# Kernel tuning notes

Measured on AMD Instinct MI355X. Metric: run time of the kernel, lower is better.

The kernel has to match this reference:

```python
import jax, jax.numpy as jnp
import numpy as np

N_NODES = 100000
N_EDGES = 1600000
D = 64
N_LAYERS = 5
N_GRAPHS = 256


def setup_inputs() -> dict:
    key = jax.random.key(0)
    ks = jax.random.split(key, 12)
    x = jax.random.normal(ks[0], (N_NODES, D), dtype=jnp.float32)
    edge_index = jax.random.randint(ks[1], (2, N_EDGES), 0, N_NODES, dtype=jnp.int64)
    batch = jnp.sort(jax.random.randint(ks[2], (N_NODES,), 0, N_GRAPHS, dtype=jnp.int64))
    s = 1.0 / np.sqrt(D)
    # stacked GINConv MLP params: Linear(D,D) -> ReLU -> Linear(D,D), per layer
    Ws1 = jax.random.uniform(ks[3], (N_LAYERS, D, D), jnp.float32, -s, s)
    bs1 = jax.random.uniform(ks[4], (N_LAYERS, D), jnp.float32, -s, s)
    Ws2 = jax.random.uniform(ks[5], (N_LAYERS, D, D), jnp.float32, -s, s)
    bs2 = jax.random.uniform(ks[6], (N_LAYERS, D), jnp.float32, -s, s)
    # final readout MLP: Linear(D,D) -> ReLU -> Linear(D,D)
    mW1 = jax.random.uniform(ks[7], (D, D), jnp.float32, -s, s)
    mb1 = jax.random.uniform(ks[8], (D,), jnp.float32, -s, s)
    mW2 = jax.random.uniform(ks[9], (D, D), jnp.float32, -s, s)
    mb2 = jax.random.uniform(ks[10], (D,), jnp.float32, -s, s)
    return {"x": x, "edge_index": edge_index, "batch": batch,
            "Ws1": Ws1, "bs1": bs1, "Ws2": Ws2, "bs2": bs2,
            "mW1": mW1, "mb1": mb1, "mW2": mW2, "mb2": mb2}


def reference(x, edge_index, batch, Ws1, bs1, Ws2, bs2, mW1, mb1, mW2, mb2):
    src, dst = edge_index[0], edge_index[1]
    h = x
    for l in range(N_LAYERS):
        # GINConv (eps=0): MLP(h + sum_{j in N(i)} h_j)
        agg = jax.ops.segment_sum(h[src], dst, num_segments=N_NODES)
        z = h + agg
        z = jax.nn.relu(z @ Ws1[l] + bs1[l])
        h = z @ Ws2[l] + bs2[l]
    # global mean pool over graphs
    sums = jax.ops.segment_sum(h, batch, num_segments=N_GRAPHS)
    cnts = jax.ops.segment_sum(jnp.ones((h.shape[0],), h.dtype), batch, num_segments=N_GRAPHS)
    pooled = sums / jnp.maximum(cnts, 1.0)[:, None]
    # readout MLP
    out = jax.nn.relu(pooled @ mW1 + mb1) @ mW2 + mb2
    return out
```

## Files before the change

kernel.cpp:

```cpp
#include <hip/hip_runtime.h>
#include <hip/hip_bf16.h>

#define N_NODES 100000
#define N_EDGES 1600000
#define DIM 64
#define N_LAYERS 5
#define N_GRAPHS 256

#define NB2 391
#define BSH 8
#define BMSK 255
#define SUBCAP2 4608
#define CAP2 6400
#define DUMMY N_NODES
#define TILE 3200
#define NTILE 500
#define MTILES (N_NODES / 16)

#define CVT_BLOCKS 6250
#define PREPACK_BLOCKS 40
#define SETUP_BLOCKS (CVT_BLOCKS + PREPACK_BLOCKS + 1)

typedef __attribute__((ext_vector_type(8))) short short8;
typedef __attribute__((ext_vector_type(4))) float float4v;

__device__ __forceinline__ unsigned short f2bf(float f) {
    unsigned int u = __float_as_uint(f);
    unsigned int r = (u + 0x7fffu + ((u >> 16) & 1u)) >> 16;
    return (unsigned short)r;
}
__device__ __forceinline__ float bf2f(unsigned short b) {
    return __uint_as_float(((unsigned int)b) << 16);
}

__global__ __launch_bounds__(256) void setup_kernel(
    const float4* __restrict__ x, ushort4* __restrict__ hb,
    const float* __restrict__ Ws1, const float* __restrict__ Ws2,
    unsigned short* __restrict__ wpk, int* __restrict__ bcursor,
    unsigned short* __restrict__ hA, unsigned short* __restrict__ hB) {
    const int b = blockIdx.x;
    const int tid = threadIdx.x;
    if (b < CVT_BLOCKS) {
        int i = b * 256 + tid;
        float4 v = x[i];
        ushort4 o;
        o.x = f2bf(v.x); o.y = f2bf(v.y); o.z = f2bf(v.z); o.w = f2bf(v.w);
        hb[i] = o;
    } else if (b < CVT_BLOCKS + PREPACK_BLOCKS) {
        int t = (b - CVT_BLOCKS) * 256 + tid;
        int lane = t & 63;
        int frag = (t >> 6) & 31;
        int l = t >> 11;
        int kf = frag & 1;
        int nt = (frag >> 1) & 3;
        int split = (frag >> 3) & 1;
        int mat = (frag >> 4) & 1;
        const float* W = (mat ? Ws2 : Ws1) + (size_t)l * DIM * DIM;
        unsigned short outv[8];
#pragma unroll
        for (int j = 0; j < 8; ++j) {
            int k = kf * 32 + ((lane >> 4) << 3) + j;
            int n = nt * 16 + (lane & 15);
            float v = W[k * DIM + n];
            unsigned short hi = f2bf(v);
            outv[j] = split ? f2bf(v - bf2f(hi)) : hi;
        }
        ushort4* dst = (ushort4*)(wpk + ((size_t)(l * 32 + frag) * 64 + lane) * 8);
        dst[0] = make_ushort4(outv[0], outv[1], outv[2], outv[3]);
        dst[1] = make_ushort4(outv[4], outv[5], outv[6], outv[7]);
    } else {
        for (int l = tid; l < NB2; l += 256) bcursor[l] = 0;
        if (tid < DIM) {
            hA[(size_t)DUMMY * DIM + tid] = 0;
            hB[(size_t)DUMMY * DIM + tid] = 0;
        }
    }
}

__global__ __launch_bounds__(256) void bin_kernel(
    const int* __restrict__ src, const int* __restrict__ dst,
    int* __restrict__ bcursor, int* __restrict__ pairbuf) {
    __shared__ int hcnt[NB2];
    __shared__ int gbase[NB2];
    __shared__ int lcur[NB2];
    const int tid = threadIdx.x;
    const int base = blockIdx.x * TILE;

    for (int l = tid; l < NB2; l += 256) { hcnt[l] = 0; lcur[l] = 0; }
    __syncthreads();
    for (int j = tid; j < TILE; j += 256) {
        int d = dst[base + j];
        atomicAdd(&hcnt[d >> BSH], 1);
    }
    __syncthreads();
    for (int l = tid; l < NB2; l += 256)
        gbase[l] = atomicAdd(&bcursor[l], hcnt[l]);
    __syncthreads();
    for (int j = tid; j < TILE; j += 256) {
        int s = src[base + j];
        int d = dst[base + j];
        int b = d >> BSH;
        int r = atomicAdd(&lcur[b], 1);
        int pos = gbase[b] + r;
        if (pos < SUBCAP2) pairbuf[b * SUBCAP2 + pos] = (s << BSH) | (d & BMSK);
    }
}

__global__ __launch_bounds__(512) void csr_kernel(
    const int* __restrict__ bcursor, const int* __restrict__ pairbuf,
    int* __restrict__ esrc, int2* __restrict__ meta) {
    __shared__ int lcnt[256];
    __shared__ int loff[256];
    __shared__ int lcur[256];
    __shared__ int s2[256];
    const int b = blockIdx.x;
    const int tid = threadIdx.x;
    int ec = bcursor[b];
    if (ec > SUBCAP2) ec = SUBCAP2;
    const int* pp = pairbuf + b * SUBCAP2;

    if (tid < 256) lcnt[tid] = 0;
    __syncthreads();
    for (int j = tid; j < ec; j += 512) atomicAdd(&lcnt[pp[j] & BMSK], 1);
    __syncthreads();

    if (tid < 256) s2[tid] = (lcnt[tid] + 7) & ~7;
    __syncthreads();
    for (int off = 1; off < 256; off <<= 1) {
        int v = (tid >= off && tid < 256) ? s2[tid - off] : 0;
        __syncthreads();
        if (tid < 256) s2[tid] += v;
        __syncthreads();
    }
    if (tid < 256) {
        int c = (lcnt[tid] + 7) & ~7;
        int exc = s2[tid] - c;
        loff[tid] = exc;
        lcur[tid] = exc;
    }
    __syncthreads();

    int* eb = esrc + (size_t)b * CAP2;
    for (int l = tid; l < 256; l += 512) {
        int st = loff[l];
        int cn = lcnt[l];
        int cp = (cn + 7) & ~7;
        int node = b * 256 + l;
        if (node < N_NODES) meta[node] = make_int2(b * CAP2 + st, cp);
        for (int j = cn; j < cp; ++j) eb[st + j] = DUMMY;
    }
    __syncthreads();

    for (int j = tid; j < ec; j += 512) {
        int p = pp[j];
        int pos = atomicAdd(&lcur[p & BMSK], 1);
        eb[pos] = p >> BSH;
    }
}

__device__ __forceinline__ void acc8(float* acc, uint4 v) {
    acc[0] += __uint_as_float(v.x << 16);
    acc[1] += __uint_as_float(v.x & 0xffff0000u);
    acc[2] += __uint_as_float(v.y << 16);
    acc[3] += __uint_as_float(v.y & 0xffff0000u);
    acc[4] += __uint_as_float(v.z << 16);
    acc[5] += __uint_as_float(v.z & 0xffff0000u);
    acc[6] += __uint_as_float(v.w << 16);
    acc[7] += __uint_as_float(v.w & 0xffff0000u);
}

typedef const __attribute__((address_space(1))) void* as1cv;
typedef __attribute__((address_space(3))) void* as3v;
__device__ __forceinline__ void gload16(const void* g, void* l) {
    __builtin_amdgcn_global_load_lds((as1cv)g, (as3v)l, 16, 0, 0);
}

__global__ __launch_bounds__(256) void agg_kernel(
    const unsigned short* __restrict__ hin, unsigned short* __restrict__ z,
    const int2* __restrict__ meta, const int* __restrict__ esrc, int n_nodes) {
    __shared__ char scratch[4][4096];
    const int lane = threadIdx.x & 63;
    const int wv = threadIdx.x >> 6;
    const int grp = lane >> 3;
    const int sub = lane & 7;
    const int wave_id = (blockIdx.x * blockDim.x + threadIdx.x) >> 6;
    const int n_waves = (gridDim.x * blockDim.x) >> 6;
    char* ring = scratch[wv];
    const char* hb = (const char*)hin;

    for (int ii = wave_id; 2 * ii < n_nodes; ii += n_waves) {
        const int iA = 2 * ii;
        const int iB = iA + 1;
        const int2 mA = meta[iA];
        const int2 mB = meta[iB];
        const float selfA = bf2f(hin[(size_t)iA * DIM + lane]);
        const float selfB = bf2f(hin[(size_t)iB * DIM + lane]);
        const int nA = mA.y, nB = mB.y;
        const int* eA = esrc + mA.x + grp;
        const int* eB = esrc + mB.x + grp;
        const int nb = ((nA > nB) ? nA : nB) >> 3;

        float accA[8] = {0.f, 0.f, 0.f, 0.f, 0.f, 0.f, 0.f, 0.f};
        float accB[8] = {0.f, 0.f, 0.f, 0.f, 0.f, 0.f, 0.f, 0.f};

        if (nb > 0) {
            int o;
            o = (0 < nA) ? 0 : 0;
            int ia0 = eA[o]; ia0 = (0 < nA) ? ia0 : DUMMY;
            int ib0 = eB[o]; ib0 = (0 < nB) ? ib0 : DUMMY;
            o = (8 < nA) ? 8 : 0;
            int ia1 = eA[o]; ia1 = (8 < nA) ? ia1 : DUMMY;
            o = (8 < nB) ? 8 : 0;
            int ib1 = eB[o]; ib1 = (8 < nB) ? ib1 : DUMMY;
            asm volatile("s_waitcnt lgkmcnt(0)" ::: "memory");
            gload16(hb + ((size_t)(unsigned)ia0 << 7) + (sub << 4), ring);
            gload16(hb + ((size_t)(unsigned)ib0 << 7) + (sub << 4), ring + 2048);
            if (nb > 1) {
                gload16(hb + ((size_t)(unsigned)ia1 << 7) + (sub << 4), ring + 1024);
                gload16(hb + ((size_t)(unsigned)ib1 << 7) + (sub << 4), ring + 3072);
            }
            asm volatile("" ::: "memory");
            int t8 = 16;
            int oA = (t8 < nA) ? t8 : 0;
            int oB = (t8 < nB) ? t8 : 0;
            int nxA = eA[oA]; nxA = (t8 < nA) ? nxA : DUMMY;
            int nxB = eB[oB]; nxB = (t8 < nB) ? nxB : DUMMY;

            for (int b = 0; b < nb; ++b) {
                if (b + 1 < nb) asm volatile("s_waitcnt vmcnt(4)" ::: "memory");
                else            asm volatile("s_waitcnt vmcnt(2)" ::: "memory");
                const int s = (b & 1) << 10;
                uint4 va = *(const uint4*)(ring + s + lane * 16);
                uint4 vb = *(const uint4*)(ring + 2048 + s + lane * 16);
                acc8(accA, va);
                acc8(accB, vb);
                if (b + 2 < nb) {
                    asm volatile("s_waitcnt lgkmcnt(0)" ::: "memory");
                    gload16(hb + ((size_t)(unsigned)nxA << 7) + (sub << 4), ring + s);
                    gload16(hb + ((size_t)(unsigned)nxB << 7) + (sub << 4), ring + 2048 + s);
                    asm volatile("" ::: "memory");
                    t8 = 8 * (b + 3);
                    oA = (t8 < nA) ? t8 : 0;
                    oB = (t8 < nB) ? t8 : 0;
                    nxA = eA[oA]; nxA = (t8 < nA) ? nxA : DUMMY;
                    nxB = eB[oB]; nxB = (t8 < nB) ? nxB : DUMMY;
                }
            }
        }

        float* zbA = (float*)ring;
        float* zbB = (float*)(ring + 2048);
        *((float4*)&zbA[grp * 64 + sub * 8 + 0]) = make_float4(accA[0], accA[1], accA[2], accA[3]);
        *((float4*)&zbA[grp * 64 + sub * 8 + 4]) = make_float4(accA[4], accA[5], accA[6], accA[7]);
        *((float4*)&zbB[grp * 64 + sub * 8 + 0]) = make_float4(accB[0], accB[1], accB[2], accB[3]);
        *((float4*)&zbB[grp * 64 + sub * 8 + 4]) = make_float4(accB[4], accB[5], accB[6], accB[7]);
        __builtin_amdgcn_wave_barrier();
        float zA = selfA, zB = selfB;
#pragma unroll
        for (int g = 0; g < 8; ++g) {
            zA += zbA[g * 64 + lane];
            zB += zbB[g * 64 + lane];
        }
        z[(size_t)iA * DIM + lane] = f2bf(zA);
        z[(size_t)iB * DIM + lane] = f2bf(zB);
        __builtin_amdgcn_wave_barrier();
    }
}

__device__ __forceinline__ short8 load_frag(const unsigned short* __restrict__ wl, int frag, int lane) {
    union { uint4 u; short8 s; } c;
    c.u = *(const uint4*)(wl + ((size_t)(frag * 64 + lane)) * 8);
    return c.s;
}

__device__ __forceinline__ void split8(const float* v, short8& hi, short8& lo) {
#pragma unroll
    for (int j = 0; j < 8; ++j) {
        unsigned short h = f2bf(v[j]);
        hi[j] = (short)h;
        lo[j] = (short)f2bf(v[j] - bf2f(h));
    }
}

__global__ __launch_bounds__(256) void mlp_mfma_kernel(
    const unsigned short* __restrict__ z, unsigned short* __restrict__ hout,
    const unsigned short* __restrict__ wl,
    const float* __restrict__ b1, const float* __restrict__ b2) {
    __shared__ float tbuf[4][16][68];
    const int lane = threadIdx.x & 63;
    const int wv = threadIdx.x >> 6;
    const int m = lane & 15;
    const int quad = lane >> 4;
    const int wave_id = (blockIdx.x * blockDim.x + threadIdx.x) >> 6;
    const int n_waves = (gridDim.x * blockDim.x) >> 6;

    float b1v[4], b2v[4];
#pragma unroll
    for (int nt = 0; nt < 4; ++nt) {
        b1v[nt] = b1[nt * 16 + m];
        b2v[nt] = b2[nt * 16 + m];
    }

    for (int tile = wave_id; tile < MTILES; tile += n_waves) {
        const int node0 = tile * 16;

        short8 a1[2];
#pragma unroll
        for (int kf = 0; kf < 2; ++kf) {
            union { uint4 u; short8 s; } c;
            c.u = *(const uint4*)(z + ((size_t)(node0 + m)) * DIM + kf * 32 + quad * 8);
            a1[kf] = c.s;
        }

        float4v acc1[4] = {};
#pragma unroll
        for (int nt = 0; nt < 4; ++nt) {
#pragma unroll
            for (int kf = 0; kf < 2; ++kf) {
                short8 bhi = load_frag(wl, ((0 * 2 + 0) * 4 + nt) * 2 + kf, lane);
                short8 blo = load_frag(wl, ((0 * 2 + 1) * 4 + nt) * 2 + kf, lane);
                acc1[nt] = __builtin_amdgcn_mfma_f32_16x16x32_bf16(a1[kf], bhi, acc1[nt], 0, 0, 0);
                acc1[nt] = __builtin_amdgcn_mfma_f32_16x16x32_bf16(a1[kf], blo, acc1[nt], 0, 0, 0);
            }
        }

#pragma unroll
        for (int nt = 0; nt < 4; ++nt) {
#pragma unroll
            for (int r = 0; r < 4; ++r) {
                float tv = acc1[nt][r] + b1v[nt];
                tbuf[wv][quad * 4 + r][nt * 16 + m] = fmaxf(tv, 0.f);
            }
        }
        __builtin_amdgcn_wave_barrier();

        short8 a2hi[2], a2lo[2];
#pragma unroll
        for (int kf = 0; kf < 2; ++kf) {
            const float4* tp = (const float4*)&tbuf[wv][m][kf * 32 + quad * 8];
            float4 t0 = tp[0];
            float4 t1 = tp[1];
            float v[8] = {t0.x, t0.y, t0.z, t0.w, t1.x, t1.y, t1.z, t1.w};
            split8(v, a2hi[kf], a2lo[kf]);
        }
        __builtin_amdgcn_wave_barrier();

        float4v acc2[4] = {};
#pragma unroll
        for (int nt = 0; nt < 4; ++nt) {
#pragma unroll
            for (int kf = 0; kf < 2; ++kf) {
                short8 bhi = load_frag(wl, ((1 * 2 + 0) * 4 + nt) * 2 + kf, lane);
                short8 blo = load_frag(wl, ((1 * 2 + 1) * 4 + nt) * 2 + kf, lane);
                acc2[nt] = __builtin_amdgcn_mfma_f32_16x16x32_bf16(a2hi[kf], bhi, acc2[nt], 0, 0, 0);
                acc2[nt] = __builtin_amdgcn_mfma_f32_16x16x32_bf16(a2hi[kf], blo, acc2[nt], 0, 0, 0);
                acc2[nt] = __builtin_amdgcn_mfma_f32_16x16x32_bf16(a2lo[kf], bhi, acc2[nt], 0, 0, 0);
            }
        }

#pragma unroll
        for (int nt = 0; nt < 4; ++nt) {
#pragma unroll
            for (int r = 0; r < 4; ++r) {
                float o = acc2[nt][r] + b2v[nt];
                hout[((size_t)(node0 + quad * 4 + r)) * DIM + nt * 16 + m] = f2bf(o);
            }
        }
    }
}

__global__ __launch_bounds__(256) void pool_mlp_kernel(
    const unsigned short* __restrict__ h, const int* __restrict__ batch,
    const float* __restrict__ mW1, const float* __restrict__ mb1,
    const float* __restrict__ mW2, const float* __restrict__ mb2,
    float* __restrict__ out, int n_nodes) {
    __shared__ float part[4][DIM];
    const int g = blockIdx.x;
    const int lane = threadIdx.x & 63;
    const int w = threadIdx.x >> 6;

    int lo = 0, hi = n_nodes;
    while (lo < hi) {
        int mid = (lo + hi) >> 1;
        if (batch[mid] < g) lo = mid + 1; else hi = mid;
    }
    const int s0 = lo;
    hi = n_nodes;
    while (lo < hi) {
        int mid = (lo + hi) >> 1;
        if (batch[mid] < g + 1) lo = mid + 1; else hi = mid;
    }
    const int e0 = lo;

    float acc = 0.f;
    int i = s0 + w;
    for (; i + 12 < e0; i += 16) {
        float v0 = bf2f(h[i * DIM + lane]);
        float v1 = bf2f(h[(i + 4) * DIM + lane]);
        float v2 = bf2f(h[(i + 8) * DIM + lane]);
        float v3 = bf2f(h[(i + 12) * DIM + lane]);
        acc += (v0 + v1) + (v2 + v3);
    }
    for (; i < e0; i += 4) acc += bf2f(h[i * DIM + lane]);
    part[w][lane] = acc;
    __syncthreads();

    if (w == 0) {
        acc = (part[0][lane] + part[1][lane]) + (part[2][lane] + part[3][lane]);
        float cntf = (float)(e0 - s0);
        acc /= fmaxf(cntf, 1.f);

        float t = mb1[lane];
#pragma unroll
        for (int d = 0; d < DIM; ++d) {
            float zd = __shfl(acc, d);
            t = fmaf(zd, mW1[d * DIM + lane], t);
        }
        t = fmaxf(t, 0.f);
        float o = mb2[lane];
#pragma unroll
        for (int d = 0; d < DIM; ++d) {
            float rd = __shfl(t, d);
            o = fmaf(rd, mW2[d * DIM + lane], o);
        }
        out[g * DIM + lane] = o;
    }
}

extern "C" void kernel_launch(void* const* d_in, const int* in_sizes, int n_in,
                              void* d_out, int out_size, void* d_ws, size_t ws_size,
                              hipStream_t stream) {
    const float* x   = (const float*)d_in[0];
    const int*   ei  = (const int*)d_in[1];
    const int*   bat = (const int*)d_in[2];
    const float* Ws1 = (const float*)d_in[3];
    const float* bs1 = (const float*)d_in[4];
    const float* Ws2 = (const float*)d_in[5];
    const float* bs2 = (const float*)d_in[6];
    const float* mW1 = (const float*)d_in[7];
    const float* mb1 = (const float*)d_in[8];
    const float* mW2 = (const float*)d_in[9];
    const float* mb2 = (const float*)d_in[10];
    float* out = (float*)d_out;

    char* ws = (char*)d_ws;
    size_t off = 0;
    auto alloc = [&](size_t bytes) {
        void* p = ws + off;
        off += (bytes + 255) & ~(size_t)255;
        return p;
    };
    int*  esrc    = (int*)alloc((size_t)NB2 * CAP2 * 4);
    int2* meta    = (int2*)alloc((size_t)N_NODES * 8);
    unsigned short* hbfA = (unsigned short*)alloc(((size_t)N_NODES + 1) * DIM * 2);
    unsigned short* hbfB = (unsigned short*)alloc(((size_t)N_NODES + 1) * DIM * 2);
    int*  bcursor = (int*)alloc((size_t)NB2 * 4);
    unsigned short* wpk = (unsigned short*)alloc((size_t)N_LAYERS * 32 * 64 * 8 * 2);
    int*   pairbuf = (int*)alloc((size_t)NB2 * SUBCAP2 * 4);
    unsigned short* zbig = (unsigned short*)alloc((size_t)N_NODES * DIM * 2);

    const int* src = ei;
    const int* dst = ei + N_EDGES;

    setup_kernel<<<SETUP_BLOCKS, 256, 0, stream>>>(
        (const float4*)x, (ushort4*)hbfA, Ws1, Ws2, wpk, bcursor, hbfA, hbfB);

    bin_kernel<<<NTILE, 256, 0, stream>>>(src, dst, bcursor, pairbuf);
    csr_kernel<<<NB2, 512, 0, stream>>>(bcursor, pairbuf, esrc, meta);

    const unsigned short* hin = hbfA;
    unsigned short* hout = hbfB;
    for (int l = 0; l < N_LAYERS; ++l) {
        agg_kernel<<<2048, 256, 0, stream>>>(hin, zbig, meta, esrc, N_NODES);
        mlp_mfma_kernel<<<2048, 256, 0, stream>>>(zbig, hout,
                                                  wpk + (size_t)l * 32 * 64 * 8,
                                                  bs1 + (size_t)l * DIM,
                                                  bs2 + (size_t)l * DIM);
        hin = hout;
        hout = (hout == hbfA) ? hbfB : hbfA;
    }
    pool_mlp_kernel<<<N_GRAPHS, 256, 0, stream>>>(hin, bat, mW1, mb1, mW2, mb2, out, N_NODES);
}
```

Baseline: 371.4 us.

## Fuse neighbor aggregation and GIN MLP into one per-wave kernel

Merges the aggregation kernel and the MFMA MLP kernel into a single kernel. Each wave aggregates 16 nodes into an XOR-swizzled LDS tile and then runs both linear layers on it, so the bf16 z buffer no longer round-trips through global memory and one launch per layer is dropped. The LDS layout for the intermediate ReLU buffer is also swizzled instead of padded. The trade-off is that gather latency and MFMA work are now serialized inside each wave, the grid shrinks to 1536 blocks, and register pressure is higher, which may reduce occupancy for the latency-bound gather.

Result: slower. 484.4 us (+30.4%).

```diff
diff --git a/kernel.cpp b/kernel.cpp
--- a/kernel.cpp
+++ b/kernel.cpp
@@ -175,124 +175,39 @@
     __builtin_amdgcn_global_load_lds((as1cv)g, (as3v)l, 16, 0, 0);
 }
 
-__global__ __launch_bounds__(256) void agg_kernel(
-    const unsigned short* __restrict__ hin, unsigned short* __restrict__ z,
-    const int2* __restrict__ meta, const int* __restrict__ esrc, int n_nodes) {
-    __shared__ char scratch[4][4096];
+__device__ __forceinline__ short8 load_frag(const unsigned short* __restrict__ wl, int frag, int lane) {
+    union { uint4 u; short8 s; } c;
+    c.u = *(const uint4*)(wl + ((size_t)(frag * 64 + lane)) * 8);
+    return c.s;
+}
+
+__device__ __forceinline__ void split8(const float* v, short8& hi, short8& lo) {
+#pragma unroll
+    for (int j = 0; j < 8; ++j) {
+        unsigned short h = f2bf(v[j]);
+        hi[j] = (short)h;
+        lo[j] = (short)f2bf(v[j] - bf2f(h));
+    }
+}
+
+__global__ __launch_bounds__(256) void fused_wave_kernel(
+    const unsigned short* __restrict__ hin, unsigned short* __restrict__ hout,
+    const int2* __restrict__ meta, const int* __restrict__ esrc,
+    const unsigned short* __restrict__ wl,
+    const float* __restrict__ b1, const float* __restrict__ b2) {
+    __shared__ char ringbuf[4][4096];
+    __shared__ unsigned short ztbuf[4][16 * DIM];
     const int lane = threadIdx.x & 63;
     const int wv = threadIdx.x >> 6;
     const int grp = lane >> 3;
     const int sub = lane & 7;
-    const int wave_id = (blockIdx.x * blockDim.x + threadIdx.x) >> 6;
-    const int n_waves = (gridDim.x * blockDim.x) >> 6;
-    char* ring = scratch[wv];
-    const char* hb = (const char*)hin;
-
-    for (int ii = wave_id; 2 * ii < n_nodes; ii += n_waves) {
-        const int iA = 2 * ii;
-        const int iB = iA + 1;
-        const int2 mA = meta[iA];
-        const int2 mB = meta[iB];
-        const float selfA = bf2f(hin[(size_t)iA * DIM + lane]);
-        const float selfB = bf2f(hin[(size_t)iB * DIM + lane]);
-        const int nA = mA.y, nB = mB.y;
-        const int* eA = esrc + mA.x + grp;
-        const int* eB = esrc + mB.x + grp;
-        const int nb = ((nA > nB) ? nA : nB) >> 3;
-
-        float accA[8] = {0.f, 0.f, 0.f, 0.f, 0.f, 0.f, 0.f, 0.f};
-        float accB[8] = {0.f, 0.f, 0.f, 0.f, 0.f, 0.f, 0.f, 0.f};
-
-        if (nb > 0) {
-            int o;
-            o = (0 < nA) ? 0 : 0;
-            int ia0 = eA[o]; ia0 = (0 < nA) ? ia0 : DUMMY;
-            int ib0 = eB[o]; ib0 = (0 < nB) ? ib0 : DUMMY;
-            o = (8 < nA) ? 8 : 0;
-            int ia1 = eA[o]; ia1 = (8 < nA) ? ia1 : DUMMY;
-            o = (8 < nB) ? 8 : 0;
-            int ib1 = eB[o]; ib1 = (8 < nB) ? ib1 : DUMMY;
-            asm volatile("s_waitcnt lgkmcnt(0)" ::: "memory");
-            gload16(hb + ((size_t)(unsigned)ia0 << 7) + (sub << 4), ring);
-            gload16(hb + ((size_t)(unsigned)ib0 << 7) + (sub << 4), ring + 2048);
-            if (nb > 1) {
-                gload16(hb + ((size_t)(unsigned)ia1 << 7) + (sub << 4), ring + 1024);
-                gload16(hb + ((size_t)(unsigned)ib1 << 7) + (sub << 4), ring + 3072);
-            }
-            asm volatile("" ::: "memory");
-            int t8 = 16;
-            int oA = (t8 < nA) ? t8 : 0;
-            int oB = (t8 < nB) ? t8 : 0;
-            int nxA = eA[oA]; nxA = (t8 < nA) ? nxA : DUMMY;
-            int nxB = eB[oB]; nxB = (t8 < nB) ? nxB : DUMMY;
-
-            for (int b = 0; b < nb; ++b) {
-                if (b + 1 < nb) asm volatile("s_waitcnt vmcnt(4)" ::: "memory");
-                else            asm volatile("s_waitcnt vmcnt(2)" ::: "memory");
-                const int s = (b & 1) << 10;
-                uint4 va = *(const uint4*)(ring + s + lane * 16);
-                uint4 vb = *(const uint4*)(ring + 2048 + s + lane * 16);
-                acc8(accA, va);
-                acc8(accB, vb);
-                if (b + 2 < nb) {
-                    asm volatile("s_waitcnt lgkmcnt(0)" ::: "memory");
-                    gload16(hb + ((size_t)(unsigned)nxA << 7) + (sub << 4), ring + s);
-                    gload16(hb + ((size_t)(unsigned)nxB << 7) + (sub << 4), ring + 2048 + s);
-                    asm volatile("" ::: "memory");
-                    t8 = 8 * (b + 3);
-                    oA = (t8 < nA) ? t8 : 0;
-                    oB = (t8 < nB) ? t8 : 0;
-                    nxA = eA[oA]; nxA = (t8 < nA) ? nxA : DUMMY;
-                    nxB = eB[oB]; nxB = (t8 < nB) ? nxB : DUMMY;
-                }
-            }
-        }
-
-        float* zbA = (float*)ring;
-        float* zbB = (float*)(ring + 2048);
-        *((float4*)&zbA[grp * 64 + sub * 8 + 0]) = make_float4(accA[0], accA[1], accA[2], accA[3]);
-        *((float4*)&zbA[grp * 64 + sub * 8 + 4]) = make_float4(accA[4], accA[5], accA[6], accA[7]);
-        *((float4*)&zbB[grp * 64 + sub * 8 + 0]) = make_float4(accB[0], accB[1], accB[2], accB[3]);
-        *((float4*)&zbB[grp * 64 + sub * 8 + 4]) = make_float4(accB[4], accB[5], accB[6], accB[7]);
-        __builtin_amdgcn_wave_barrier();
-        float zA = selfA, zB = selfB;
-#pragma unroll
-        for (int g = 0; g < 8; ++g) {
-            zA += zbA[g * 64 + lane];
-            zB += zbB[g * 64 + lane];
-        }
-        z[(size_t)iA * DIM + lane] = f2bf(zA);
-        z[(size_t)iB * DIM + lane] = f2bf(zB);
-        __builtin_amdgcn_wave_barrier();
-    }
-}
-
-__device__ __forceinline__ short8 load_frag(const unsigned short* __restrict__ wl, int frag, int lane) {
-    union { uint4 u; short8 s; } c;
-    c.u = *(const uint4*)(wl + ((size_t)(frag * 64 + lane)) * 8);
-    return c.s;
-}
-
-__device__ __forceinline__ void split8(const float* v, short8& hi, short8& lo) {
-#pragma unroll
-    for (int j = 0; j < 8; ++j) {
-        unsigned short h = f2bf(v[j]);
-        hi[j] = (short)h;
-        lo[j] = (short)f2bf(v[j] - bf2f(h));
-    }
-}
-
-__global__ __launch_bounds__(256) void mlp_mfma_kernel(
-    const unsigned short* __restrict__ z, unsigned short* __restrict__ hout,
-    const unsigned short* __restrict__ wl,
-    const float* __restrict__ b1, const float* __restrict__ b2) {
-    __shared__ float tbuf[4][16][68];
-    const int lane = threadIdx.x & 63;
-    const int wv = threadIdx.x >> 6;
     const int m = lane & 15;
     const int quad = lane >> 4;
     const int wave_id = (blockIdx.x * blockDim.x + threadIdx.x) >> 6;
     const int n_waves = (gridDim.x * blockDim.x) >> 6;
+    char* ring = ringbuf[wv];
+    unsigned short* zt = ztbuf[wv];
+    const char* hb = (const char*)hin;
 
     float b1v[4], b2v[4];
 #pragma unroll
@@ -304,65 +219,141 @@
     for (int tile = wave_id; tile < MTILES; tile += n_waves) {
         const int node0 = tile * 16;
 
-        short8 a1[2];
+        for (int p = 0; p < 8; ++p) {
+            const int iA = node0 + 2 * p;
+            const int iB = iA + 1;
+            const int2 mA = meta[iA];
+            const int2 mB = meta[iB];
+            const float selfA = bf2f(hin[(size_t)iA * DIM + lane]);
+            const float selfB = bf2f(hin[(size_t)iB * DIM + lane]);
+            const int nA = mA.y, nB = mB.y;
+            const int* eA = esrc + mA.x + grp;
+            const int* eB = esrc + mB.x + grp;
+            const int nb = ((nA > nB) ? nA : nB) >> 3;
+
+            float accA[8] = {0.f, 0.f, 0.f, 0.f, 0.f, 0.f, 0.f, 0.f};
+            float accB[8] = {0.f, 0.f, 0.f, 0.f, 0.f, 0.f, 0.f, 0.f};
+
+            if (nb > 0) {
+                int o;
+                o = (0 < nA) ? 0 : 0;
+                int ia0 = eA[o]; ia0 = (0 < nA) ? ia0 : DUMMY;
+                int ib0 = eB[o]; ib0 = (0 < nB) ? ib0 : DUMMY;
+                o = (8 < nA) ? 8 : 0;
+                int ia1 = eA[o]; ia1 = (8 < nA) ? ia1 : DUMMY;
+                o = (8 < nB) ? 8 : 0;
+                int ib1 = eB[o]; ib1 = (8 < nB) ? ib1 : DUMMY;
+                asm volatile("s_waitcnt lgkmcnt(0)" ::: "memory");
+                gload16(hb + ((size_t)(unsigned)ia0 << 7) + (sub << 4), ring);
+                gload16(hb + ((size_t)(unsigned)ib0 << 7) + (sub << 4), ring + 2048);
+                if (nb > 1) {
+                    gload16(hb + ((size_t)(unsigned)ia1 << 7) + (sub << 4), ring + 1024);
+                    gload16(hb + ((size_t)(unsigned)ib1 << 7) + (sub << 4), ring + 3072);
+                }
+                asm volatile("" ::: "memory");
+                int t8 = 16;
+                int oA = (t8 < nA) ? t8 : 0;
+                int oB = (t8 < nB) ? t8 : 0;
+                int nxA = eA[oA]; nxA = (t8 < nA) ? nxA : DUMMY;
+                int nxB = eB[oB]; nxB = (t8 < nB) ? nxB : DUMMY;
+
+                for (int b = 0; b < nb; ++b) {
+                    if (b + 1 < nb) asm volatile("s_waitcnt vmcnt(4)" ::: "memory");
+                    else            asm volatile("s_waitcnt vmcnt(2)" ::: "memory");
+                    const int s = (b & 1) << 10;
+                    uint4 va = *(const uint4*)(ring + s + lane * 16);
+                    uint4 vb = *(const uint4*)(ring + 2048 + s + lane * 16);
+                    acc8(accA, va);
+                    acc8(accB, vb);
+                    if (b + 2 < nb) {
+                        asm volatile("s_waitcnt lgkmcnt(0)" ::: "memory");
+                        gload16(hb + ((size_t)(unsigned)nxA << 7) + (sub << 4), ring + s);
+                        gload16(hb + ((size_t)(unsigned)nxB << 7) + (sub << 4), ring + 2048 + s);
+                        asm volatile("" ::: "memory");
+                        t8 = 8 * (b + 3);
+                        oA = (t8 < nA) ? t8 : 0;
+                        oB = (t8 < nB) ? t8 : 0;
+                        nxA = eA[oA]; nxA = (t8 < nA) ? nxA : DUMMY;
+                        nxB = eB[oB]; nxB = (t8 < nB) ? nxB : DUMMY;
+                    }
+                }
+            }
+
+            float* zbA = (float*)ring;
+            float* zbB = (float*)(ring + 2048);
+            *((float4*)&zbA[grp * 64 + sub * 8 + 0]) = make_float4(accA[0], accA[1], accA[2], accA[3]);
+            *((float4*)&zbA[grp * 64 + sub * 8 + 4]) = make_float4(accA[4], accA[5], accA[6], accA[7]);
+            *((float4*)&zbB[grp * 64 + sub * 8 + 0]) = make_float4(accB[0], accB[1], accB[2], accB[3]);
+            *((float4*)&zbB[grp * 64 + sub * 8 + 4]) = make_float4(accB[4], accB[5], accB[6], accB[7]);
+            __builtin_amdgcn_wave_barrier();
+            float zA = selfA, zB = selfB;
+#pragma unroll
+            for (int g = 0; g < 8; ++g) {
+                zA += zbA[g * 64 + lane];
+                zB += zbB[g * 64 + lane];
+            }
+            const int rA = 2 * p;
+            const int rB = rA + 1;
+            zt[rA * DIM + (lane ^ ((rA & 7) << 3))] = f2bf(zA);
+            zt[rB * DIM + (lane ^ ((rB & 7) << 3))] = f2bf(zB);
+            __builtin_amdgcn_wave_barrier();
+        }
+
+        short8 a1f[2];
 #pragma unroll
         for (int kf = 0; kf < 2; ++kf) {
-            union { uint4 u; short8 s; } c;
-            c.u = *(const uint4*)(z + ((size_t)(node0 + m)) * DIM + kf * 32 + quad * 8);
-            a1[kf] = c.s;
-        }
-
-        float4v acc1[4] = {};
+            const int c = (kf * 32 + quad * 8) ^ ((m & 7) << 3);
+            union { uint4 u; short8 s; } cu;
+            cu.u = *(const uint4*)(zt + m * DIM + c);
+            a1f[kf] = cu.s;
+        }
+        float* tb = (float*)ring;
 #pragma unroll
         for (int nt = 0; nt < 4; ++nt) {
-#pragma unroll
-            for (int kf = 0; kf < 2; ++kf) {
-                short8 bhi = load_frag(wl, ((0 * 2 + 0) * 4 + nt) * 2 + kf, lane);
-                short8 blo = load_frag(wl, ((0 * 2 + 1) * 4 + nt) * 2 + kf, lane);
-                acc1[nt] = __builtin_amdgcn_mfma_f32_16x16x32_bf16(a1[kf], bhi, acc1[nt], 0, 0, 0);
-                acc1[nt] = __builtin_amdgcn_mfma_f32_16x16x32_bf16(a1[kf], blo, acc1[nt], 0, 0, 0);
+            short8 bhi0 = load_frag(wl, 0 + nt * 2 + 0, lane);
+            short8 blo0 = load_frag(wl, 8 + nt * 2 + 0, lane);
+            short8 bhi1 = load_frag(wl, 0 + nt * 2 + 1, lane);
+            short8 blo1 = load_frag(wl, 8 + nt * 2 + 1, lane);
+            float4v acc1 = {};
+            acc1 = __builtin_amdgcn_mfma_f32_16x16x32_bf16(a1f[0], bhi0, acc1, 0, 0, 0);
+            acc1 = __builtin_amdgcn_mfma_f32_16x16x32_bf16(a1f[0], blo0, acc1, 0, 0, 0);
+            acc1 = __builtin_amdgcn_mfma_f32_16x16x32_bf16(a1f[1], bhi1, acc1, 0, 0, 0);
+            acc1 = __builtin_amdgcn_mfma_f32_16x16x32_bf16(a1f[1], blo1, acc1, 0, 0, 0);
+#pragma unroll
+            for (int r = 0; r < 4; ++r) {
+                const int row = quad * 4 + r;
+                tb[row * 64 + ((nt * 16 + m) ^ ((row & 7) << 3))] = fmaxf(acc1[r] + b1v[nt], 0.f);
             }
         }
+        __builtin_amdgcn_wave_barrier();
+
+        short8 a2hi[2], a2lo[2];
+#pragma unroll
+        for (int kf = 0; kf < 2; ++kf) {
+            const int c = (kf * 32 + quad * 8) ^ ((m & 7) << 3);
+            float v[8];
+            *(float4*)(v + 0) = *(const float4*)(tb + m * 64 + c + 0);
+            *(float4*)(v + 4) = *(const float4*)(tb + m * 64 + c + 4);
+            split8(v, a2hi[kf], a2lo[kf]);
+        }
+        __builtin_amdgcn_wave_barrier();
 
 #pragma unroll
         for (int nt = 0; nt < 4; ++nt) {
+            short8 bhi0 = load_frag(wl, 16 + nt * 2 + 0, lane);
+            short8 blo0 = load_frag(wl, 24 + nt * 2 + 0, lane);
+            short8 bhi1 = load_frag(wl, 16 + nt * 2 + 1, lane);
+            short8 blo1 = load_frag(wl, 24 + nt * 2 + 1, lane);
+            float4v acc2 = {};
+            acc2 = __builtin_amdgcn_mfma_f32_16x16x32_bf16(a2hi[0], bhi0, acc2, 0, 0, 0);
+            acc2 = __builtin_amdgcn_mfma_f32_16x16x32_bf16(a2hi[0], blo0, acc2, 0, 0, 0);
+            acc2 = __builtin_amdgcn_mfma_f32_16x16x32_bf16(a2lo[0], bhi0, acc2, 0, 0, 0);
+            acc2 = __builtin_amdgcn_mfma_f32_16x16x32_bf16(a2hi[1], bhi1, acc2, 0, 0, 0);
+            acc2 = __builtin_amdgcn_mfma_f32_16x16x32_bf16(a2hi[1], blo1, acc2, 0, 0, 0);
+            acc2 = __builtin_amdgcn_mfma_f32_16x16x32_bf16(a2lo[1], bhi1, acc2, 0, 0, 0);
 #pragma unroll
             for (int r = 0; r < 4; ++r) {
-                float tv = acc1[nt][r] + b1v[nt];
-                tbuf[wv][quad * 4 + r][nt * 16 + m] = fmaxf(tv, 0.f);
-            }
-        }
-        __builtin_amdgcn_wave_barrier();
-
-        short8 a2hi[2], a2lo[2];
-#pragma unroll
-        for (int kf = 0; kf < 2; ++kf) {
-            const float4* tp = (const float4*)&tbuf[wv][m][kf * 32 + quad * 8];
-            float4 t0 = tp[0];
-            float4 t1 = tp[1];
-            float v[8] = {t0.x, t0.y, t0.z, t0.w, t1.x, t1.y, t1.z, t1.w};
-            split8(v, a2hi[kf], a2lo[kf]);
-        }
-        __builtin_amdgcn_wave_barrier();
-
-        float4v acc2[4] = {};
-#pragma unroll
-        for (int nt = 0; nt < 4; ++nt) {
-#pragma unroll
-            for (int kf = 0; kf < 2; ++kf) {
-                short8 bhi = load_frag(wl, ((1 * 2 + 0) * 4 + nt) * 2 + kf, lane);
-                short8 blo = load_frag(wl, ((1 * 2 + 1) * 4 + nt) * 2 + kf, lane);
-                acc2[nt] = __builtin_amdgcn_mfma_f32_16x16x32_bf16(a2hi[kf], bhi, acc2[nt], 0, 0, 0);
-                acc2[nt] = __builtin_amdgcn_mfma_f32_16x16x32_bf16(a2hi[kf], blo, acc2[nt], 0, 0, 0);
-                acc2[nt] = __builtin_amdgcn_mfma_f32_16x16x32_bf16(a2lo[kf], bhi, acc2[nt], 0, 0, 0);
-            }
-        }
-
-#pragma unroll
-        for (int nt = 0; nt < 4; ++nt) {
-#pragma unroll
-            for (int r = 0; r < 4; ++r) {
-                float o = acc2[nt][r] + b2v[nt];
+                float o = acc2[r] + b2v[nt];
                 hout[((size_t)(node0 + quad * 4 + r)) * DIM + nt * 16 + m] = f2bf(o);
             }
         }
@@ -457,7 +448,6 @@
     int*  bcursor = (int*)alloc((size_t)NB2 * 4);
     unsigned short* wpk = (unsigned short*)alloc((size_t)N_LAYERS * 32 * 64 * 8 * 2);
     int*   pairbuf = (int*)alloc((size_t)NB2 * SUBCAP2 * 4);
-    unsigned short* zbig = (unsigned short*)alloc((size_t)N_NODES * DIM * 2);
 
     const int* src = ei;
     const int* dst = ei + N_EDGES;
@@ -471,11 +461,10 @@
     const unsigned short* hin = hbfA;
     unsigned short* hout = hbfB;
     for (int l = 0; l < N_LAYERS; ++l) {
-        agg_kernel<<<2048, 256, 0, stream>>>(hin, zbig, meta, esrc, N_NODES);
-        mlp_mfma_kernel<<<2048, 256, 0, stream>>>(zbig, hout,
-                                                  wpk + (size_t)l * 32 * 64 * 8,
-                                                  bs1 + (size_t)l * DIM,
-                                                  bs2 + (size_t)l * DIM);
+        fused_wave_kernel<<<1536, 256, 0, stream>>>(hin, hout, meta, esrc,
+                                                    wpk + (size_t)l * 32 * 64 * 8,
+                                                    bs1 + (size_t)l * DIM,
+                                                    bs2 + (size_t)l * DIM);
         hin = hout;
         hout = (hout == hbfA) ? hbfB : hbfA;
     }
```
